# Kernel optimization log

Hardware: AMD Instinct MI355X
Metric: run time of the kernel (lower is better)

Reference implementation:

```python
import jax, jax.numpy as jnp
import numpy as np

WEIGHT_THRESH = 0.0
EPS = 1e-5


def setup_inputs() -> dict:
    key = jax.random.key(0)
    k1, k2, k3 = jax.random.split(key, 3)
    B, N = 8192, 1024
    src_points = jax.random.normal(k1, (B, N, 3), dtype=jnp.float32)
    tgt_points = jax.random.normal(k2, (B, N, 3), dtype=jnp.float32)
    weights = jax.random.uniform(k3, (B, N), dtype=jnp.float32)
    return {"src_points": src_points, "tgt_points": tgt_points, "weights": weights}


def reference(src_points, tgt_points, weights):
    # Threshold and normalize weights: (B, N)
    w = jnp.where(weights < WEIGHT_THRESH, jnp.zeros_like(weights), weights)
    w = w / (jnp.sum(w, axis=1, keepdims=True) + EPS)
    w3 = w[..., None]  # (B, N, 1)

    # Weighted centroids: (B, 1, 3)
    src_centroid = jnp.sum(src_points * w3, axis=1, keepdims=True)
    tgt_centroid = jnp.sum(tgt_points * w3, axis=1, keepdims=True)

    src_c = src_points - src_centroid
    tgt_c = tgt_points - tgt_centroid

    # Weighted covariance H = src_c^T @ (w * tgt_c): (B, 3, 3)
    H = jnp.einsum('bnc,bnd->bcd', src_c, w3 * tgt_c)

    # torch.svd returns U, S, V with H = U S V^T; jnp returns U, S, Vh
    U, _, Vh = jnp.linalg.svd(H)
    V = jnp.swapaxes(Vh, -1, -2)
    Ut = jnp.swapaxes(U, -1, -2)

    # Reflection correction: E = diag(1, 1, sign(det(V @ Ut)))
    s = jnp.sign(jnp.linalg.det(jnp.matmul(V, Ut)))  # (B,)
    d = jnp.stack([jnp.ones_like(s), jnp.ones_like(s), s], axis=-1)  # (B, 3)
    R = jnp.matmul(V, Ut * d[..., None])  # V @ diag(d) @ Ut, (B, 3, 3)

    # Translation: t = tgt_centroid - R @ src_centroid, (B, 3)
    t = tgt_centroid[:, 0, :] - jnp.einsum('bij,bj->bi', R, src_centroid[:, 0, :])

    # Assemble 4x4 transform
    B = src_points.shape[0]
    top = jnp.concatenate([R, t[..., None]], axis=-1)  # (B, 3, 4)
    bottom = jnp.broadcast_to(
        jnp.array([[0.0, 0.0, 0.0, 1.0]], dtype=R.dtype), (B, 1, 4)
    )
    transform = jnp.concatenate([top, bottom], axis=1)  # (B, 4, 4)
    return transform
```

## Files before the change

### kernel.cpp

```cpp
#include <hip/hip_runtime.h>
#include <math.h>

#define TPB 256
#define NPTS 1024

template<int P, int Q, int R>
__device__ __forceinline__ void jrot(float a[3][3], float V[3][3]) {
  float apq = a[P][Q];
  if (fabsf(apq) < 1e-30f) return;
  float theta = (a[Q][Q] - a[P][P]) / (2.0f * apq);
  float t = copysignf(1.0f, theta) / (fabsf(theta) + sqrtf(theta * theta + 1.0f));
  float c = 1.0f / sqrtf(t * t + 1.0f);
  float s = t * c;
  float app = a[P][P], aqq = a[Q][Q];
  a[P][P] = app - t * apq;
  a[Q][Q] = aqq + t * apq;
  a[P][Q] = 0.0f; a[Q][P] = 0.0f;
  float arp = a[R][P], arq = a[R][Q];
  a[R][P] = c * arp - s * arq; a[P][R] = a[R][P];
  a[R][Q] = s * arp + c * arq; a[Q][R] = a[R][Q];
#pragma unroll
  for (int i = 0; i < 3; ++i) {
    float vip = V[i][P], viq = V[i][Q];
    V[i][P] = c * vip - s * viq;
    V[i][Q] = s * vip + c * viq;
  }
}

#define CSWAP(I, J)                                                        \
  if (ev[I] < ev[J]) {                                                     \
    float e_ = ev[I]; ev[I] = ev[J]; ev[J] = e_;                           \
    _Pragma("unroll")                                                      \
    for (int r2_ = 0; r2_ < 3; ++r2_) {                                    \
      float v_ = V[r2_][I]; V[r2_][I] = V[r2_][J]; V[r2_][J] = v_;         \
    }                                                                      \
  }

__device__ __forceinline__ void svd_tail_write(const float r[16], float* o) {
  const float S = r[0];
  const float inv = 1.0f / (S + 1e-5f);
  const float sc[3] = {r[1] * inv, r[2] * inv, r[3] * inv};
  const float tc[3] = {r[4] * inv, r[5] * inv, r[6] * inv};
  const float f = 2.0f - S * inv;

  float H[3][3];
#pragma unroll
  for (int c = 0; c < 3; ++c)
#pragma unroll
    for (int d = 0; d < 3; ++d)
      H[c][d] = r[7 + 3 * c + d] * inv - sc[c] * tc[d] * f;

  float Bm[3][3];
#pragma unroll
  for (int i = 0; i < 3; ++i)
#pragma unroll
    for (int j = 0; j < 3; ++j)
      Bm[i][j] = H[0][i] * H[0][j] + H[1][i] * H[1][j] + H[2][i] * H[2][j];

  float V[3][3] = {{1, 0, 0}, {0, 1, 0}, {0, 0, 1}};
  for (int sweep = 0; sweep < 8; ++sweep) {
    jrot<0, 1, 2>(Bm, V);
    jrot<0, 2, 1>(Bm, V);
    jrot<1, 2, 0>(Bm, V);
  }
  float ev[3] = {Bm[0][0], Bm[1][1], Bm[2][2]};
  CSWAP(0, 1)
  CSWAP(1, 2)
  CSWAP(0, 1)

  float U[3][3];
  float w0[3], w1[3];
#pragma unroll
  for (int i = 0; i < 3; ++i)
    w0[i] = H[i][0] * V[0][0] + H[i][1] * V[1][0] + H[i][2] * V[2][0];
  float n0 = sqrtf(w0[0] * w0[0] + w0[1] * w0[1] + w0[2] * w0[2]);
  float in0 = (n0 > 1e-20f) ? 1.0f / n0 : 0.0f;
#pragma unroll
  for (int i = 0; i < 3; ++i) U[i][0] = w0[i] * in0;

#pragma unroll
  for (int i = 0; i < 3; ++i)
    w1[i] = H[i][0] * V[0][1] + H[i][1] * V[1][1] + H[i][2] * V[2][1];
  float d01 = U[0][0] * w1[0] + U[1][0] * w1[1] + U[2][0] * w1[2];
#pragma unroll
  for (int i = 0; i < 3; ++i) w1[i] -= d01 * U[i][0];
  float n1 = sqrtf(w1[0] * w1[0] + w1[1] * w1[1] + w1[2] * w1[2]);
  float in1 = (n1 > 1e-20f) ? 1.0f / n1 : 0.0f;
#pragma unroll
  for (int i = 0; i < 3; ++i) U[i][1] = w1[i] * in1;

  U[0][2] = U[1][0] * U[2][1] - U[2][0] * U[1][1];
  U[1][2] = U[2][0] * U[0][1] - U[0][0] * U[2][1];
  U[2][2] = U[0][0] * U[1][1] - U[1][0] * U[0][1];

  float detV = V[0][0] * (V[1][1] * V[2][2] - V[1][2] * V[2][1]) -
               V[0][1] * (V[1][0] * V[2][2] - V[1][2] * V[2][0]) +
               V[0][2] * (V[1][0] * V[2][1] - V[1][1] * V[2][0]);
  float s3 = (detV >= 0.0f) ? 1.0f : -1.0f;

  float R[3][3];
#pragma unroll
  for (int i = 0; i < 3; ++i)
#pragma unroll
    for (int j = 0; j < 3; ++j)
      R[i][j] = V[i][0] * U[j][0] + V[i][1] * U[j][1] + s3 * V[i][2] * U[j][2];

  float tr[3];
#pragma unroll
  for (int i = 0; i < 3; ++i)
    tr[i] = tc[i] - (R[i][0] * sc[0] + R[i][1] * sc[1] + R[i][2] * sc[2]);

  o[0] = R[0][0]; o[1] = R[0][1]; o[2]  = R[0][2]; o[3]  = tr[0];
  o[4] = R[1][0]; o[5] = R[1][1]; o[6]  = R[1][2]; o[7]  = tr[1];
  o[8] = R[2][0]; o[9] = R[2][1]; o[10] = R[2][2]; o[11] = tr[2];
  o[12] = 0.0f;   o[13] = 0.0f;   o[14] = 0.0f;    o[15] = 1.0f;
}

template<bool FUSED>
__global__ __launch_bounds__(TPB) void wproc_main(
    const float* __restrict__ src, const float* __restrict__ tgt,
    const float* __restrict__ wts, float* __restrict__ out,
    float* __restrict__ ws) {
  const int b = blockIdx.x;
  const int t = threadIdx.x;
  const int lane = t & 63, wave = t >> 6;

  __shared__ float sh_part[64][20];
  __shared__ float sh_fin[4][17];
  __shared__ float sh_r[16];

  const float4* g_src = (const float4*)(src + (size_t)b * (NPTS * 3));
  const float4* g_tgt = (const float4*)(tgt + (size_t)b * (NPTS * 3));
  const float4* g_w   = (const float4*)(wts + (size_t)b * NPTS);

  const float4 s0 = g_src[3 * t + 0], s1 = g_src[3 * t + 1], s2 = g_src[3 * t + 2];
  const float4 u0 = g_tgt[3 * t + 0], u1 = g_tgt[3 * t + 1], u2 = g_tgt[3 * t + 2];
  const float4 w4 = g_w[t];

  float acc[16];
#pragma unroll
  for (int k = 0; k < 16; ++k) acc[k] = 0.0f;

#define PT(W, SX, SY, SZ, TX, TY, TZ)                                   \
  {                                                                     \
    float wv = fmaxf((W), 0.0f);               \
    float wsx = wv * (SX), wsy = wv * (SY), wsz = wv * (SZ);            \
    acc[0] += wv;                                                       \
    acc[1] += wsx;       acc[2] += wsy;       acc[3] += wsz;            \
    acc[4] += wv * (TX); acc[5] += wv * (TY); acc[6] += wv * (TZ);      \
    acc[7]  += wsx * (TX); acc[8]  += wsx * (TY); acc[9]  += wsx * (TZ);\
    acc[10] += wsy * (TX); acc[11] += wsy * (TY); acc[12] += wsy * (TZ);\
    acc[13] += wsz * (TX); acc[14] += wsz * (TY); acc[15] += wsz * (TZ);\
  }

  PT(w4.x, s0.x, s0.y, s0.z, u0.x, u0.y, u0.z)
  PT(w4.y, s0.w, s1.x, s1.y, u0.w, u1.x, u1.y)
  PT(w4.z, s1.z, s1.w, s2.x, u1.z, u1.w, u2.x)
  PT(w4.w, s2.y, s2.z, s2.w, u2.y, u2.z, u2.w)
#undef PT

#pragma unroll
  for (int k = 0; k < 16; ++k) acc[k] += __shfl_down(acc[k], 32, 64);
#pragma unroll
  for (int k = 0; k < 16; ++k) acc[k] += __shfl_down(acc[k], 16, 64);

  if (lane < 16) {
    float4* pr = (float4*)&sh_part[wave * 16 + lane][0];
    pr[0] = make_float4(acc[0], acc[1], acc[2], acc[3]);
    pr[1] = make_float4(acc[4], acc[5], acc[6], acc[7]);
    pr[2] = make_float4(acc[8], acc[9], acc[10], acc[11]);
    pr[3] = make_float4(acc[12], acc[13], acc[14], acc[15]);
  }
  __syncthreads();

  if (t < 64) {
    const int k = t & 15, g = t >> 4;
    float s = 0.0f;
#pragma unroll
    for (int j = 0; j < 16; ++j) s += sh_part[g * 16 + j][k];
    sh_fin[g][k] = s;
  }
  __syncthreads();

  if (t < 16) {
    float rk = sh_fin[0][t] + sh_fin[1][t] + sh_fin[2][t] + sh_fin[3][t];
    if constexpr (FUSED) sh_r[t] = rk;
    else ws[(size_t)b * 16 + t] = rk;
  }

  if constexpr (FUSED) {
    __syncthreads();
    if (t != 0) return;
    float r[16];
#pragma unroll
    for (int k = 0; k < 16; ++k) r[k] = sh_r[k];
    svd_tail_write(r, out + (size_t)b * 16);
  }
}

__global__ __launch_bounds__(TPB) void wproc_svd(
    const float* __restrict__ ws, float* __restrict__ out, int B) {
  const int i = blockIdx.x * TPB + threadIdx.x;
  if (i >= B) return;
  const float4* p = (const float4*)(ws + (size_t)i * 16);
  const float4 a = p[0], bq = p[1], c = p[2], d = p[3];
  const float r[16] = {a.x,  a.y,  a.z,  a.w,  bq.x, bq.y, bq.z, bq.w,
                       c.x,  c.y,  c.z,  c.w,  d.x,  d.y,  d.z,  d.w};
  svd_tail_write(r, out + (size_t)i * 16);
}

extern "C" void kernel_launch(void* const* d_in, const int* in_sizes, int n_in,
                              void* d_out, int out_size, void* d_ws, size_t ws_size,
                              hipStream_t stream) {
  const float* src = (const float*)d_in[0];
  const float* tgt = (const float*)d_in[1];
  const float* wts = (const float*)d_in[2];
  float* out = (float*)d_out;
  const int B = in_sizes[0] / (NPTS * 3);
  const size_t need = (size_t)B * 16 * sizeof(float);
  if (ws_size >= need) {
    wproc_main<false><<<dim3(B), dim3(TPB), 0, stream>>>(src, tgt, wts, out,
                                                         (float*)d_ws);
    wproc_svd<<<dim3((B + TPB - 1) / TPB), dim3(TPB), 0, stream>>>(
        (const float*)d_ws, out, B);
  } else {
    wproc_main<true><<<dim3(B), dim3(TPB), 0, stream>>>(src, tgt, wts, out,
                                                        nullptr);
  }
}
```

Measured before the change: 238.8 us.

## Fuse SVD tail into main kernel and stage point loads through LDS

Replaces the two-kernel path (reduction then a separate batched SVD kernel) with one fused kernel where thread 0 of each block runs the 3x3 SVD. Global loads of src/tgt become fully coalesced float4 reads staged through shared memory before each thread reads its strided 3-float4 chunk. It also adds an occupancy hint to launch bounds and vectorises the output store. This removes a kernel launch and a workspace round trip, but leaves a serial single-thread SVD tail per block and adds LDS traffic plus extra barriers.

```diff
diff --git a/kernel.cpp b/kernel.cpp
--- a/kernel.cpp
+++ b/kernel.cpp
@@ -110,32 +110,39 @@
   for (int i = 0; i < 3; ++i)
     tr[i] = tc[i] - (R[i][0] * sc[0] + R[i][1] * sc[1] + R[i][2] * sc[2]);
 
-  o[0] = R[0][0]; o[1] = R[0][1]; o[2]  = R[0][2]; o[3]  = tr[0];
-  o[4] = R[1][0]; o[5] = R[1][1]; o[6]  = R[1][2]; o[7]  = tr[1];
-  o[8] = R[2][0]; o[9] = R[2][1]; o[10] = R[2][2]; o[11] = tr[2];
-  o[12] = 0.0f;   o[13] = 0.0f;   o[14] = 0.0f;    o[15] = 1.0f;
-}
-
-template<bool FUSED>
-__global__ __launch_bounds__(TPB) void wproc_main(
+  float4* o4 = (float4*)o;
+  o4[0] = make_float4(R[0][0], R[0][1], R[0][2], tr[0]);
+  o4[1] = make_float4(R[1][0], R[1][1], R[1][2], tr[1]);
+  o4[2] = make_float4(R[2][0], R[2][1], R[2][2], tr[2]);
+  o4[3] = make_float4(0.0f, 0.0f, 0.0f, 1.0f);
+}
+
+__global__ __launch_bounds__(TPB, 6) void wproc_fused(
     const float* __restrict__ src, const float* __restrict__ tgt,
-    const float* __restrict__ wts, float* __restrict__ out,
-    float* __restrict__ ws) {
+    const float* __restrict__ wts, float* __restrict__ out) {
   const int b = blockIdx.x;
   const int t = threadIdx.x;
   const int lane = t & 63, wave = t >> 6;
 
-  __shared__ float sh_part[64][20];
+  __shared__ float4 sh_src[NPTS * 3 / 4];
+  __shared__ float4 sh_tgt[NPTS * 3 / 4];
   __shared__ float sh_fin[4][17];
   __shared__ float sh_r[16];
+  float(*sh_part)[20] = (float(*)[20]) sh_src;
 
   const float4* g_src = (const float4*)(src + (size_t)b * (NPTS * 3));
   const float4* g_tgt = (const float4*)(tgt + (size_t)b * (NPTS * 3));
   const float4* g_w   = (const float4*)(wts + (size_t)b * NPTS);
 
-  const float4 s0 = g_src[3 * t + 0], s1 = g_src[3 * t + 1], s2 = g_src[3 * t + 2];
-  const float4 u0 = g_tgt[3 * t + 0], u1 = g_tgt[3 * t + 1], u2 = g_tgt[3 * t + 2];
+  const float4 a0 = g_src[t], a1 = g_src[t + 256], a2 = g_src[t + 512];
+  const float4 c0 = g_tgt[t], c1 = g_tgt[t + 256], c2 = g_tgt[t + 512];
   const float4 w4 = g_w[t];
+  sh_src[t] = a0; sh_src[t + 256] = a1; sh_src[t + 512] = a2;
+  sh_tgt[t] = c0; sh_tgt[t + 256] = c1; sh_tgt[t + 512] = c2;
+  __syncthreads();
+
+  const float4 s0 = sh_src[3 * t + 0], s1 = sh_src[3 * t + 1], s2 = sh_src[3 * t + 2];
+  const float4 u0 = sh_tgt[3 * t + 0], u1 = sh_tgt[3 * t + 1], u2 = sh_tgt[3 * t + 2];
 
   float acc[16];
 #pragma unroll
@@ -164,6 +171,8 @@
 #pragma unroll
   for (int k = 0; k < 16; ++k) acc[k] += __shfl_down(acc[k], 16, 64);
 
+  __syncthreads();
+
   if (lane < 16) {
     float4* pr = (float4*)&sh_part[wave * 16 + lane][0];
     pr[0] = make_float4(acc[0], acc[1], acc[2], acc[3]);
@@ -182,31 +191,15 @@
   }
   __syncthreads();
 
-  if (t < 16) {
-    float rk = sh_fin[0][t] + sh_fin[1][t] + sh_fin[2][t] + sh_fin[3][t];
-    if constexpr (FUSED) sh_r[t] = rk;
-    else ws[(size_t)b * 16 + t] = rk;
-  }
-
-  if constexpr (FUSED) {
-    __syncthreads();
-    if (t != 0) return;
-    float r[16];
-#pragma unroll
-    for (int k = 0; k < 16; ++k) r[k] = sh_r[k];
-    svd_tail_write(r, out + (size_t)b * 16);
-  }
-}
-
-__global__ __launch_bounds__(TPB) void wproc_svd(
-    const float* __restrict__ ws, float* __restrict__ out, int B) {
-  const int i = blockIdx.x * TPB + threadIdx.x;
-  if (i >= B) return;
-  const float4* p = (const float4*)(ws + (size_t)i * 16);
-  const float4 a = p[0], bq = p[1], c = p[2], d = p[3];
-  const float r[16] = {a.x,  a.y,  a.z,  a.w,  bq.x, bq.y, bq.z, bq.w,
-                       c.x,  c.y,  c.z,  c.w,  d.x,  d.y,  d.z,  d.w};
-  svd_tail_write(r, out + (size_t)i * 16);
+  if (t < 16)
+    sh_r[t] = sh_fin[0][t] + sh_fin[1][t] + sh_fin[2][t] + sh_fin[3][t];
+  __syncthreads();
+
+  if (t != 0) return;
+  float r[16];
+#pragma unroll
+  for (int k = 0; k < 16; ++k) r[k] = sh_r[k];
+  svd_tail_write(r, out + (size_t)b * 16);
 }
 
 extern "C" void kernel_launch(void* const* d_in, const int* in_sizes, int n_in,
@@ -217,14 +210,5 @@
   const float* wts = (const float*)d_in[2];
   float* out = (float*)d_out;
   const int B = in_sizes[0] / (NPTS * 3);
-  const size_t need = (size_t)B * 16 * sizeof(float);
-  if (ws_size >= need) {
-    wproc_main<false><<<dim3(B), dim3(TPB), 0, stream>>>(src, tgt, wts, out,
-                                                         (float*)d_ws);
-    wproc_svd<<<dim3((B + TPB - 1) / TPB), dim3(TPB), 0, stream>>>(
-        (const float*)d_ws, out, B);
-  } else {
-    wproc_main<true><<<dim3(B), dim3(TPB), 0, stream>>>(src, tgt, wts, out,
-                                                        nullptr);
-  }
-}
+  wproc_fused<<<dim3(B), dim3(TPB), 0, stream>>>(src, tgt, wts, out);
+}
```

Result: slower. 244.7 us (+2.5%).
